# Optimization experiments

Measured on AMD Instinct MI355X. Metric: run time of the kernel, lower is better.

## Reference

```python
import jax, jax.numpy as jnp
import numpy as np

CROP_H, CROP_W = 14, 14
MAX_BS = 64  # max boxes per image per level (MoldBatch padding)
NUM_LEVELS = 4


def _crop_and_resize(fmap, boxes, box_indices, ch, cw):
    """Bilinear tf.image.crop_and_resize equivalent.
    fmap: [B,H,W,C]; boxes: [N,4] normalized (y1,x1,y2,x2); box_indices: [N] int32.
    Returns [N,ch,cw,C]; samples outside the image get extrapolation value 0."""
    B, H, W, C = fmap.shape
    y1, x1, y2, x2 = boxes[:, 0], boxes[:, 1], boxes[:, 2], boxes[:, 3]
    ty = jnp.arange(ch, dtype=boxes.dtype) / (ch - 1)
    tx = jnp.arange(cw, dtype=boxes.dtype) / (cw - 1)
    ys = y1[:, None] * (H - 1) + ty[None, :] * ((y2 - y1)[:, None] * (H - 1))  # [N,ch]
    xs = x1[:, None] * (W - 1) + tx[None, :] * ((x2 - x1)[:, None] * (W - 1))  # [N,cw]
    y0f = jnp.floor(ys); x0f = jnp.floor(xs)
    wy = (ys - y0f)[:, :, None, None]  # [N,ch,1,1]
    wx = (xs - x0f)[:, None, :, None]  # [N,1,cw,1]
    y0 = jnp.clip(y0f.astype(jnp.int32), 0, H - 1); y1i = jnp.clip(y0 + 1, 0, H - 1)
    x0 = jnp.clip(x0f.astype(jnp.int32), 0, W - 1); x1i = jnp.clip(x0 + 1, 0, W - 1)
    bi = box_indices[:, None, None]
    g = lambda yi, xi: fmap[bi, yi[:, :, None], xi[:, None, :], :]  # [N,ch,cw,C]
    top = g(y0, x0) * (1 - wx) + g(y0, x1i) * wx
    bot = g(y1i, x0) * (1 - wx) + g(y1i, x1i) * wx
    out = top * (1 - wy) + bot * wy
    valid = ((ys >= 0) & (ys <= H - 1))[:, :, None] & ((xs >= 0) & (xs <= W - 1))[:, None, :]
    return out * valid[..., None].astype(out.dtype)


def setup_inputs() -> dict:
    key = jax.random.key(0)
    ks = jax.random.split(key, 8)
    B, N, C = 4, 128, 256
    sizes = [256, 128, 64, 32]
    inp = {}
    for i, s in enumerate(sizes):
        inp[f"fmap{i}"] = jax.random.normal(ks[i], (B, s, s, C), dtype=jnp.float32)
    ids = jax.random.randint(ks[4], (B, N), 0, NUM_LEVELS).astype(jnp.float32)
    cxy = jax.random.uniform(ks[5], (B, N, 2), minval=0.0, maxval=1024.0)
    wh = jax.random.uniform(ks[6], (B, N, 2), minval=16.0, maxval=256.0)
    cls_id = jnp.zeros((B, N, 1), jnp.float32)
    conf = jnp.full((B, N, 1), 0.9, jnp.float32)
    inp["dist_boxes"] = jnp.concatenate([ids[..., None], cxy, wh, cls_id, conf], axis=-1)
    inp["images"] = jnp.zeros((B, 1024, 1024, 3), jnp.float32)
    return inp


def _forward(fmaps, dist_boxes, images):
    B, N, _ = dist_boxes.shape
    Hi, Wi = images.shape[1], images.shape[2]
    cx, cy, w, h = (dist_boxes[..., 1], dist_boxes[..., 2], dist_boxes[..., 3], dist_boxes[..., 4])
    # NormalizeBoxes: (cx,cy,w,h) pixels -> normalized (y1,x1,y2,x2) for crop_and_resize
    norm_boxes = jnp.stack([
        (cy - h / 2) / (Hi - 1), (cx - w / 2) / (Wi - 1),
        (cy + h / 2) / (Hi - 1), (cx + w / 2) / (Wi - 1)], axis=-1)  # [B,N,4]
    ids = dist_boxes[..., 0]
    flat_boxes = norm_boxes.reshape(B * N, 4)
    box_idx = jnp.repeat(jnp.arange(B, dtype=jnp.int32), N)
    b_idx = jnp.broadcast_to(jnp.arange(B)[:, None], (B, N))
    boxes6 = dist_boxes[..., 1:]  # [B,N,6]
    roi_fmaps, roi_boxes = [], []
    for lvl, fmap in enumerate(fmaps):
        C = fmap.shape[-1]
        mask = ids == lvl  # [B,N] level routing (tf.where/gather_nd equivalent)
        crops = _crop_and_resize(fmap, flat_boxes, box_idx, CROP_H, CROP_W)
        crops = crops.reshape(B, N, CROP_H, CROP_W, C)
        # MoldBatch: scatter level-l boxes densely per image, zero-padded to MAX_BS
        rank = jnp.cumsum(mask.astype(jnp.int32), axis=1) - 1
        dest = jnp.where(mask & (rank < MAX_BS), rank, MAX_BS)  # overflow -> dump slot
        pf = jnp.zeros((B, MAX_BS + 1, CROP_H, CROP_W, C), crops.dtype)
        pf = pf.at[b_idx, dest].set(crops * mask[..., None, None, None].astype(crops.dtype))
        roi_fmaps.append(pf[:, :MAX_BS])
        pb = jnp.zeros((B, MAX_BS + 1, 6), dist_boxes.dtype)
        pb = pb.at[b_idx, dest].set(boxes6 * mask[..., None].astype(boxes6.dtype))
        roi_boxes.append(pb[:, :MAX_BS])
    return jnp.stack(roi_fmaps), jnp.concatenate(roi_boxes, axis=1)


def reference(fmap0, fmap1, fmap2, fmap3, dist_boxes, images):
    return _forward([fmap0, fmap1, fmap2, fmap3], dist_boxes, images)
```

## Files before the change

### kernel.cpp

```cpp
#include <hip/hip_runtime.h>

#define CROP 14
#define MAXBS 64
#define NLVL 4
#define BDIM 4
#define NBOX 128
#define CCH 256

__global__ void roi_meta_kernel(const float* __restrict__ db,
                                int* __restrict__ slot_map,
                                float* __restrict__ out1) {
    int b = blockIdx.x;
    int t = threadIdx.x;
    __shared__ int lvl_arr[NBOX];
    __shared__ int smap[NLVL * MAXBS];

    if (t < NBOX) {
        lvl_arr[t] = (int)db[(b * NBOX + t) * 7 + 0];
    }
    smap[t] = -1;
    __syncthreads();

    if (t < NLVL) {
        int r = 0;
        for (int n = 0; n < NBOX; ++n) {
            if (lvl_arr[n] == t) {
                if (r < MAXBS) smap[t * MAXBS + r] = n;
                r++;
            }
        }
    }
    __syncthreads();

    int n = smap[t];
    int lvl = t >> 6;
    int slot = t & 63;
    slot_map[(lvl * BDIM + b) * MAXBS + slot] = n;

    float* o = out1 + ((size_t)(b * (NLVL * MAXBS) + t)) * 6;
    if (n >= 0) {
        const float* src = db + (b * NBOX + n) * 7 + 1;
        #pragma unroll
        for (int j = 0; j < 6; ++j) o[j] = src[j];
    } else {
        #pragma unroll
        for (int j = 0; j < 6; ++j) o[j] = 0.f;
    }
}

__global__ void roi_crop_kernel(const float* __restrict__ f0,
                                const float* __restrict__ f1,
                                const float* __restrict__ f2,
                                const float* __restrict__ f3,
                                const float* __restrict__ db,
                                const int* __restrict__ slot_map,
                                float* __restrict__ out0) {
    int bid = blockIdx.x;
    int y  = bid % CROP;
    int sl = bid / CROP;
    int c  = threadIdx.x;

    float* out = out0 + ((size_t)(sl * CROP + y)) * CROP * CCH;

    int n = slot_map[sl];
    if (n < 0) {
        #pragma unroll
        for (int x = 0; x < CROP; ++x) out[x * CCH + c] = 0.f;
        return;
    }

    int lvl = sl >> 8;
    int b   = (sl >> 6) & 3;
    int s   = 256 >> lvl;
    const float* f = (lvl == 0) ? f0 : (lvl == 1) ? f1 : (lvl == 2) ? f2 : f3;

    const float* bx = db + (b * NBOX + n) * 7;
    float cx = bx[1], cy = bx[2], w = bx[3], h = bx[4];

    float y1n = (cy - h * 0.5f) / 1023.0f;
    float x1n = (cx - w * 0.5f) / 1023.0f;
    float y2n = (cy + h * 0.5f) / 1023.0f;
    float x2n = (cx + w * 0.5f) / 1023.0f;

    float Hm1 = (float)(s - 1);
    float ty = (float)y / 13.0f;
    float ys = y1n * Hm1 + ty * ((y2n - y1n) * Hm1);
    float y0f = floorf(ys);
    float wy = ys - y0f;
    int iy0 = (int)y0f;
    iy0 = iy0 < 0 ? 0 : (iy0 > s - 1 ? s - 1 : iy0);
    int iy1 = iy0 + 1;
    if (iy1 > s - 1) iy1 = s - 1;
    bool vy = (ys >= 0.f) && (ys <= Hm1);

    const float* rowT = f + ((size_t)(b * s + iy0)) * s * CCH;
    const float* rowB = f + ((size_t)(b * s + iy1)) * s * CCH;

    float x1nH   = x1n * Hm1;
    float xscale = (x2n - x1n) * Hm1;
    float omwy = 1.f - wy;

    #pragma unroll
    for (int x = 0; x < CROP; ++x) {
        float xs = x1nH + ((float)x / 13.0f) * xscale;
        float x0f = floorf(xs);
        float wx = xs - x0f;
        int ix0 = (int)x0f;
        ix0 = ix0 < 0 ? 0 : (ix0 > s - 1 ? s - 1 : ix0);
        int ix1 = ix0 + 1;
        if (ix1 > s - 1) ix1 = s - 1;
        bool vx = (xs >= 0.f) && (xs <= Hm1);

        float a  = rowT[ix0 * CCH + c];
        float bv = rowT[ix1 * CCH + c];
        float cv = rowB[ix0 * CCH + c];
        float dv = rowB[ix1 * CCH + c];

        float omwx = 1.f - wx;
        float top = a  * omwx + bv * wx;
        float bot = cv * omwx + dv * wx;
        float v   = top * omwy + bot * wy;

        out[x * CCH + c] = (vy && vx) ? v : 0.f;
    }
}

extern "C" void kernel_launch(void* const* d_in, const int* in_sizes, int n_in,
                              void* d_out, int out_size, void* d_ws, size_t ws_size,
                              hipStream_t stream) {
    const float* f0 = (const float*)d_in[0];
    const float* f1 = (const float*)d_in[1];
    const float* f2 = (const float*)d_in[2];
    const float* f3 = (const float*)d_in[3];
    const float* db = (const float*)d_in[4];

    float* out0 = (float*)d_out;
    float* out1 = out0 + (size_t)NLVL * BDIM * MAXBS * CROP * CROP * CCH;
    int* slot_map = (int*)d_ws;

    roi_meta_kernel<<<BDIM, 256, 0, stream>>>(db, slot_map, out1);
    roi_crop_kernel<<<NLVL * BDIM * MAXBS * CROP, 256, 0, stream>>>(
        f0, f1, f2, f3, db, slot_map, out0);
}
```

Baseline: 463.5 us.

## Vectorize crop kernel with float4 and assign one block per ROI slot

The crop kernel now launches one block per ROI slot instead of one per slot-row. Each of the four waves handles every fourth crop row, with lanes moving float4 channel vectors for 128-bit loads and stores. This cuts the number of memory instructions and removes repeated per-block box setup. The trade-off is 14x fewer blocks (1024) with uneven work per wave: waves 0 and 1 get four rows, waves 2 and 3 get three. That may lower occupancy and latency hiding.

```diff
diff --git a/kernel.cpp b/kernel.cpp
--- a/kernel.cpp
+++ b/kernel.cpp
@@ -6,6 +6,7 @@
 #define BDIM 4
 #define NBOX 128
 #define CCH 256
+#define C4 (CCH / 4)
 
 __global__ void roi_meta_kernel(const float* __restrict__ db,
                                 int* __restrict__ slot_map,
@@ -48,31 +49,29 @@
     }
 }
 
-__global__ void roi_crop_kernel(const float* __restrict__ f0,
-                                const float* __restrict__ f1,
-                                const float* __restrict__ f2,
-                                const float* __restrict__ f3,
-                                const float* __restrict__ db,
-                                const int* __restrict__ slot_map,
-                                float* __restrict__ out0) {
-    int bid = blockIdx.x;
-    int y  = bid % CROP;
-    int sl = bid / CROP;
-    int c  = threadIdx.x;
-
-    float* out = out0 + ((size_t)(sl * CROP + y)) * CROP * CCH;
+__global__ __launch_bounds__(256) void roi_crop_kernel(
+        const float* __restrict__ f0,
+        const float* __restrict__ f1,
+        const float* __restrict__ f2,
+        const float* __restrict__ f3,
+        const float* __restrict__ db,
+        const int* __restrict__ slot_map,
+        float* __restrict__ out0) {
+    int sl = blockIdx.x;
+    float4* outb = (float4*)(out0 + (size_t)sl * (CROP * CROP * CCH));
 
     int n = slot_map[sl];
     if (n < 0) {
-        #pragma unroll
-        for (int x = 0; x < CROP; ++x) out[x * CCH + c] = 0.f;
+        float4 z = make_float4(0.f, 0.f, 0.f, 0.f);
+        for (int i = threadIdx.x; i < CROP * CROP * C4; i += 256) outb[i] = z;
         return;
     }
 
     int lvl = sl >> 8;
     int b   = (sl >> 6) & 3;
     int s   = 256 >> lvl;
-    const float* f = (lvl == 0) ? f0 : (lvl == 1) ? f1 : (lvl == 2) ? f2 : f3;
+    const float4* f = (const float4*)((lvl == 0) ? f0 : (lvl == 1) ? f1
+                                    : (lvl == 2) ? f2 : f3);
 
     const float* bx = db + (b * NBOX + n) * 7;
     float cx = bx[1], cy = bx[2], w = bx[3], h = bx[4];
@@ -82,46 +81,58 @@
     float y2n = (cy + h * 0.5f) / 1023.0f;
     float x2n = (cx + w * 0.5f) / 1023.0f;
 
-    float Hm1 = (float)(s - 1);
-    float ty = (float)y / 13.0f;
-    float ys = y1n * Hm1 + ty * ((y2n - y1n) * Hm1);
-    float y0f = floorf(ys);
-    float wy = ys - y0f;
-    int iy0 = (int)y0f;
-    iy0 = iy0 < 0 ? 0 : (iy0 > s - 1 ? s - 1 : iy0);
-    int iy1 = iy0 + 1;
-    if (iy1 > s - 1) iy1 = s - 1;
-    bool vy = (ys >= 0.f) && (ys <= Hm1);
+    float Hm1    = (float)(s - 1);
+    float ybase  = y1n * Hm1;
+    float yscale = (y2n - y1n) * Hm1;
+    float xbase  = x1n * Hm1;
+    float xscale = (x2n - x1n) * Hm1;
 
-    const float* rowT = f + ((size_t)(b * s + iy0)) * s * CCH;
-    const float* rowB = f + ((size_t)(b * s + iy1)) * s * CCH;
+    int wave = threadIdx.x >> 6;
+    int lane = threadIdx.x & 63;
 
-    float x1nH   = x1n * Hm1;
-    float xscale = (x2n - x1n) * Hm1;
-    float omwy = 1.f - wy;
+    for (int y = wave; y < CROP; y += 4) {
+        float ty = (float)y / 13.0f;
+        float ys = ybase + ty * yscale;
+        float y0f = floorf(ys);
+        float wy = ys - y0f;
+        int iy0 = (int)y0f;
+        iy0 = iy0 < 0 ? 0 : (iy0 > s - 1 ? s - 1 : iy0);
+        int iy1 = iy0 + 1;
+        if (iy1 > s - 1) iy1 = s - 1;
+        bool vy = (ys >= 0.f) && (ys <= Hm1);
 
-    #pragma unroll
-    for (int x = 0; x < CROP; ++x) {
-        float xs = x1nH + ((float)x / 13.0f) * xscale;
-        float x0f = floorf(xs);
-        float wx = xs - x0f;
-        int ix0 = (int)x0f;
-        ix0 = ix0 < 0 ? 0 : (ix0 > s - 1 ? s - 1 : ix0);
-        int ix1 = ix0 + 1;
-        if (ix1 > s - 1) ix1 = s - 1;
-        bool vx = (xs >= 0.f) && (xs <= Hm1);
+        const float4* rowT = f + ((size_t)(b * s + iy0)) * s * C4;
+        const float4* rowB = f + ((size_t)(b * s + iy1)) * s * C4;
+        float omwy = 1.f - wy;
+        float4* orow = outb + y * (CROP * C4);
 
-        float a  = rowT[ix0 * CCH + c];
-        float bv = rowT[ix1 * CCH + c];
-        float cv = rowB[ix0 * CCH + c];
-        float dv = rowB[ix1 * CCH + c];
+        #pragma unroll
+        for (int x = 0; x < CROP; ++x) {
+            float tx = (float)x / 13.0f;
+            float xs = xbase + tx * xscale;
+            float x0f = floorf(xs);
+            float wx = xs - x0f;
+            int ix0 = (int)x0f;
+            ix0 = ix0 < 0 ? 0 : (ix0 > s - 1 ? s - 1 : ix0);
+            int ix1 = ix0 + 1;
+            if (ix1 > s - 1) ix1 = s - 1;
+            bool v = vy && (xs >= 0.f) && (xs <= Hm1);
 
-        float omwx = 1.f - wx;
-        float top = a  * omwx + bv * wx;
-        float bot = cv * omwx + dv * wx;
-        float v   = top * omwy + bot * wy;
+            float4 a  = rowT[ix0 * C4 + lane];
+            float4 bb = rowT[ix1 * C4 + lane];
+            float4 cc = rowB[ix0 * C4 + lane];
+            float4 dd = rowB[ix1 * C4 + lane];
 
-        out[x * CCH + c] = (vy && vx) ? v : 0.f;
+            float omwx = 1.f - wx;
+            float4 r;
+            r.x = (a.x * omwx + bb.x * wx) * omwy + (cc.x * omwx + dd.x * wx) * wy;
+            r.y = (a.y * omwx + bb.y * wx) * omwy + (cc.y * omwx + dd.y * wx) * wy;
+            r.z = (a.z * omwx + bb.z * wx) * omwy + (cc.z * omwx + dd.z * wx) * wy;
+            r.w = (a.w * omwx + bb.w * wx) * omwy + (cc.w * omwx + dd.w * wx) * wy;
+            if (!v) r = make_float4(0.f, 0.f, 0.f, 0.f);
+
+            orow[x * C4 + lane] = r;
+        }
     }
 }
 
@@ -139,6 +150,6 @@
     int* slot_map = (int*)d_ws;
 
     roi_meta_kernel<<<BDIM, 256, 0, stream>>>(db, slot_map, out1);
-    roi_crop_kernel<<<NLVL * BDIM * MAXBS * CROP, 256, 0, stream>>>(
+    roi_crop_kernel<<<NLVL * BDIM * MAXBS, 256, 0, stream>>>(
         f0, f1, f2, f3, db, slot_map, out0);
 }
```

Result: slower. 484.4 us (+4.5%).
